# Performance work log

Hardware: AMD Instinct MI355X
Metric: run time of the kernel (lower is better)

The kernel has to match this reference:

```python
import jax, jax.numpy as jnp
import numpy as np

DELTA_V = 0.5
DELTA_D = 3.0
PARAM_VAR = 1.0
PARAM_DIST = 1.0
PARAM_REG = 0.001
NUM_BIN_LABELS = 2   # binary labels in {0,1}
NUM_INST_LABELS = 6  # background + 5 lanes


def _disc_loss_single(pred, labels, num_labels, delta_v, delta_d):
    """pred: [D, N] float, labels: [N] int in [0, num_labels).
    Assumes all labels present (true w.h.p. for large N), so
    torch.unique(sorted=True) == arange(num_labels)."""
    D, N = pred.shape
    K = num_labels
    labels = labels.astype(jnp.int32)
    ones = jnp.ones((N,), dtype=pred.dtype)
    counts = jax.ops.segment_sum(ones, labels, num_segments=K)            # [K]
    sums = jax.ops.segment_sum(pred.T, labels, num_segments=K)            # [K, D]
    means = sums / counts[:, None]                                        # [K, D] segment means

    # variance (pull) term: distance of each pixel embedding to its segment mean
    mu_expand = means[labels]                                             # [N, D]
    dist = jnp.sqrt(jnp.sum((mu_expand - pred.T) ** 2, axis=1))           # [N]
    dist = jnp.maximum(dist - delta_v, 0.0) ** 2
    var_per_label = jax.ops.segment_sum(dist, labels, num_segments=K) / counts
    l_var = jnp.mean(var_per_label)

    # distance (push) term over all ordered pairs i != j of segment means
    diff = means[:, None, :] - means[None, :, :]                          # [K, K, D]
    sq = jnp.sum(diff ** 2, axis=-1)                                      # [K, K]
    offdiag = ~jnp.eye(K, dtype=bool)
    sq_safe = jnp.where(offdiag, sq, 1.0)  # avoid sqrt(0) grad NaN on diagonal
    dn = jnp.maximum(2.0 * delta_d - jnp.sqrt(sq_safe), 0.0) ** 2
    l_dist = jnp.sum(jnp.where(offdiag, dn, 0.0)) / (K * (K - 1))

    # regularizer: mean L2 norm of segment means (norm over feature dim)
    l_reg = jnp.mean(jnp.sqrt(jnp.sum(means ** 2, axis=1)))

    return PARAM_VAR * l_var + PARAM_DIST * l_dist + PARAM_REG * l_reg


def setup_inputs() -> dict:
    key = jax.random.key(0)
    k1, k2, k3, k4 = jax.random.split(key, 4)
    B, MN = 4, 512 * 1024
    return {
        "binary_logits": jax.random.normal(k1, (B, 2, MN), dtype=jnp.float32),
        "binary_labels": jax.random.randint(k2, (B, MN), 0, NUM_BIN_LABELS, dtype=jnp.int64),
        "instance_logits": jax.random.normal(k3, (B, 5, MN), dtype=jnp.float32),
        "instance_labels": jax.random.randint(k4, (B, MN), 0, NUM_INST_LABELS, dtype=jnp.int64),
    }


def reference(binary_logits, binary_labels, instance_logits, instance_labels):
    bin_loss_per = jax.vmap(
        lambda p, l: _disc_loss_single(p, l, NUM_BIN_LABELS, DELTA_V, DELTA_D)
    )(binary_logits, binary_labels)
    inst_loss_per = jax.vmap(
        lambda p, l: _disc_loss_single(p, l, NUM_INST_LABELS, DELTA_V, DELTA_D)
    )(instance_logits, instance_labels)
    return jnp.mean(bin_loss_per), jnp.mean(inst_loss_per)
```

## Files before the change

### kernel.cpp

```cpp
#include <hip/hip_runtime.h>
#include <math.h>

#define DELTA_V 0.5f
#define DELTA_D 3.0f
#define P_REG   0.001f

#define BPS   128
#define TPB   256
#define NVMAX 36

#define P1_OFF   0
#define CNT_OFF  (8 * BPS * 36)
#define MEAN_OFF (CNT_OFF + 48)
#define LDR_OFF  (MEAN_OFF + 240)
#define P2_OFF   (LDR_OFF + 8)

template<int K, int D>
__device__ void pass1_body(const float* __restrict__ pred,
                           const int*  __restrict__ labels,
                           float* __restrict__ partials,
                           int n4, float (*lredW)[NVMAX]) {
    constexpr int NV = K * (D + 1);
    const float4* pred4 = (const float4*)pred;
    const int4*   lab4  = (const int4*)labels;

    float acc[K][D + 1];
    #pragma unroll
    for (int k = 0; k < K; ++k)
        #pragma unroll
        for (int j = 0; j <= D; ++j) acc[k][j] = 0.f;

    const int idx0   = blockIdx.x * TPB + threadIdx.x;
    const int stride = BPS * TPB;
    for (int i = idx0; i < n4; i += stride) {
        int4 lv = lab4[i];
        int labs[4] = {lv.x, lv.y, lv.z, lv.w};
        float4 xv[D];
        #pragma unroll
        for (int d = 0; d < D; ++d) xv[d] = pred4[(size_t)d * n4 + i];
        const float* xs = (const float*)&xv[0];
        #pragma unroll
        for (int c = 0; c < 4; ++c) {
            const int lab = labs[c];
            #pragma unroll
            for (int k = 0; k < K; ++k) {
                const float ind = (lab == k) ? 1.f : 0.f;
                acc[k][D] += ind;
                #pragma unroll
                for (int d = 0; d < D; ++d)
                    acc[k][d] = fmaf(ind, xs[d * 4 + c], acc[k][d]);
            }
        }
    }

    const int wave = threadIdx.x >> 6, lane = threadIdx.x & 63;
    #pragma unroll
    for (int k = 0; k < K; ++k) {
        #pragma unroll
        for (int j = 0; j <= D; ++j) {
            float v = acc[k][j];
            for (int off = 32; off > 0; off >>= 1) v += __shfl_down(v, off);
            if (lane == 0) lredW[wave][k * (D + 1) + j] = v;
        }
    }
    __syncthreads();
    if (threadIdx.x < NV) {
        const int t = threadIdx.x;
        partials[t] = lredW[0][t] + lredW[1][t] + lredW[2][t] + lredW[3][t];
    }
}

__global__ __launch_bounds__(TPB)
void pass1_fused(const float* __restrict__ bl, const int* __restrict__ bL,
                 const float* __restrict__ il, const int* __restrict__ iL,
                 float* __restrict__ ws, int MN) {
    const int s = blockIdx.y, b = s & 3;
    __shared__ float lredW[4][NVMAX];
    float* partials = ws + P1_OFF + (size_t)(s * BPS + blockIdx.x) * NVMAX;
    if (s < 4) pass1_body<2, 2>(bl + (size_t)b * 2 * MN, bL + (size_t)b * MN, partials, MN >> 2, lredW);
    else       pass1_body<6, 5>(il + (size_t)b * 5 * MN, iL + (size_t)b * MN, partials, MN >> 2, lredW);
}

__global__ void mid_kernel(float* __restrict__ ws) {
    const int s = blockIdx.x;
    const int isInst = s >> 2;
    const int K = isInst ? 6 : 2, D = isInst ? 5 : 2;
    const int NV = K * (D + 1);
    const float* P = ws + P1_OFF + (size_t)s * BPS * NVMAX;
    const int t = threadIdx.x;
    __shared__ float tot[NVMAX];
    __shared__ float muS[30];
    __shared__ float cntS[6];
    if (t < NV) {
        float v = 0.f;
        for (int j = 0; j < BPS; ++j) v += P[j * NVMAX + t];
        tot[t] = v;
        const int k = t / (D + 1), jj = t % (D + 1);
        if (jj == D) { cntS[k] = v; ws[CNT_OFF + s * 6 + k] = v; }
    }
    __syncthreads();
    if (t < NV) {
        const int k = t / (D + 1), jj = t % (D + 1);
        if (jj < D) {
            const float m = tot[t] / cntS[k];
            muS[k * D + jj] = m;
            ws[MEAN_OFF + s * 30 + k * D + jj] = m;
        }
    }
    __syncthreads();
    if (t == 0) {
        float l_dist = 0.f, l_reg = 0.f;
        for (int i = 0; i < K; ++i) {
            float n2 = 0.f;
            for (int d = 0; d < D; ++d) n2 += muS[i * D + d] * muS[i * D + d];
            l_reg += sqrtf(n2);
            for (int j = 0; j < K; ++j) {
                if (i == j) continue;
                float sq = 0.f;
                for (int d = 0; d < D; ++d) { const float df = muS[i * D + d] - muS[j * D + d]; sq += df * df; }
                const float dn = fmaxf(2.f * DELTA_D - sqrtf(sq), 0.f);
                l_dist += dn * dn;
            }
        }
        l_dist /= (float)(K * (K - 1));
        l_reg  /= (float)K;
        ws[LDR_OFF + s] = l_dist + P_REG * l_reg;
    }
}

template<int K, int D>
__device__ void pass2_body(const float* __restrict__ pred,
                           const int*  __restrict__ labels,
                           const float* __restrict__ means,
                           float* __restrict__ partials,
                           int n4, float* mu, float (*lredW)[6]) {
    if (threadIdx.x < K * D) mu[threadIdx.x] = means[threadIdx.x];
    __syncthreads();

    const float4* pred4 = (const float4*)pred;
    const int4*   lab4  = (const int4*)labels;

    float acc[K];
    #pragma unroll
    for (int k = 0; k < K; ++k) acc[k] = 0.f;

    const int idx0   = blockIdx.x * TPB + threadIdx.x;
    const int stride = BPS * TPB;
    for (int i = idx0; i < n4; i += stride) {
        int4 lv = lab4[i];
        int labs[4] = {lv.x, lv.y, lv.z, lv.w};
        float4 xv[D];
        #pragma unroll
        for (int d = 0; d < D; ++d) xv[d] = pred4[(size_t)d * n4 + i];
        const float* xs = (const float*)&xv[0];
        #pragma unroll
        for (int c = 0; c < 4; ++c) {
            const int lab = labs[c];
            float sq = 0.f;
            #pragma unroll
            for (int d = 0; d < D; ++d) {
                const float df = mu[lab * D + d] - xs[d * 4 + c];
                sq = fmaf(df, df, sq);
            }
            const float h = fmaxf(sqrtf(sq) - DELTA_V, 0.f);
            const float h2 = h * h;
            #pragma unroll
            for (int k = 0; k < K; ++k)
                acc[k] += (lab == k) ? h2 : 0.f;
        }
    }

    const int wave = threadIdx.x >> 6, lane = threadIdx.x & 63;
    #pragma unroll
    for (int k = 0; k < K; ++k) {
        float v = acc[k];
        for (int off = 32; off > 0; off >>= 1) v += __shfl_down(v, off);
        if (lane == 0) lredW[wave][k] = v;
    }
    __syncthreads();
    if (threadIdx.x < K) {
        const int t = threadIdx.x;
        partials[t] = lredW[0][t] + lredW[1][t] + lredW[2][t] + lredW[3][t];
    }
}

__global__ __launch_bounds__(TPB)
void pass2_fused(const float* __restrict__ bl, const int* __restrict__ bL,
                 const float* __restrict__ il, const int* __restrict__ iL,
                 float* __restrict__ ws, int MN) {
    const int s = blockIdx.y, b = s & 3;
    __shared__ float mu[30];
    __shared__ float lredW[4][6];
    const float* means = ws + MEAN_OFF + s * 30;
    float* partials = ws + P2_OFF + (size_t)(s * BPS + blockIdx.x) * 6;
    if (s < 4) pass2_body<2, 2>(bl + (size_t)b * 2 * MN, bL + (size_t)b * MN, means, partials, MN >> 2, mu, lredW);
    else       pass2_body<6, 5>(il + (size_t)b * 5 * MN, iL + (size_t)b * MN, means, partials, MN >> 2, mu, lredW);
}

__global__ void final_kernel(const float* __restrict__ ws, float* __restrict__ out) {
    __shared__ float contrib[48];
    const int t = threadIdx.x;
    if (t < 48) {
        const int s = t / 6, k = t % 6;
        const int Ks = (s < 4) ? 2 : 6;
        float c = 0.f;
        if (k < Ks) {
            float v = 0.f;
            for (int j = 0; j < BPS; ++j) v += ws[P2_OFF + (size_t)(s * BPS + j) * 6 + k];
            c = v / ws[CNT_OFF + s * 6 + k];
        }
        contrib[t] = c;
    }
    __syncthreads();
    if (t == 0) {
        float totB = 0.f, totI = 0.f;
        for (int s = 0; s < 8; ++s) {
            const int Ks = (s < 4) ? 2 : 6;
            float lv = 0.f;
            for (int k = 0; k < Ks; ++k) lv += contrib[s * 6 + k];
            lv /= (float)Ks;
            const float loss = lv + ws[LDR_OFF + s];
            if (s < 4) totB += loss; else totI += loss;
        }
        out[0] = totB * 0.25f;
        out[1] = totI * 0.25f;
    }
}

extern "C" void kernel_launch(void* const* d_in, const int* in_sizes, int n_in,
                              void* d_out, int out_size, void* d_ws, size_t ws_size,
                              hipStream_t stream) {
    const float* bin_logits  = (const float*)d_in[0];
    const int*   bin_labels  = (const int*)d_in[1];
    const float* inst_logits = (const float*)d_in[2];
    const int*   inst_labels = (const int*)d_in[3];
    float* ws  = (float*)d_ws;
    float* out = (float*)d_out;

    const int B  = 4;
    const int MN = in_sizes[1] / B;

    dim3 grid(BPS, 8), block(TPB);
    pass1_fused<<<grid, block, 0, stream>>>(bin_logits, bin_labels, inst_logits, inst_labels, ws, MN);
    mid_kernel<<<8, 64, 0, stream>>>(ws);
    pass2_fused<<<grid, block, 0, stream>>>(bin_logits, bin_labels, inst_logits, inst_labels, ws, MN);
    final_kernel<<<1, 64, 0, stream>>>(ws, out);
}
```

Before: 140.2 us.

## Fold mid and final reductions into passes via last-block atomic counters

Replaces the separate mid and final kernels with a last-block-done pattern. Each pass kernel increments an atomic counter, and the last block performs the cross-block reduction, which removes two small kernel launches. The grid becomes 1D and gives binary segments 64 blocks and instance segments 128 blocks, which rebalances work between the lighter and heavier segments. It adds a memset for the counters, threadfences, and an atomic per block.

```diff
diff --git a/kernel.cpp b/kernel.cpp
--- a/kernel.cpp
+++ b/kernel.cpp
@@ -5,12 +5,15 @@
 #define DELTA_D 3.0f
 #define P_REG   0.001f
 
-#define BPS   128
-#define TPB   256
-#define NVMAX 36
-
-#define P1_OFF   0
-#define CNT_OFF  (8 * BPS * 36)
+#define TPB    256
+#define BIN_B  64
+#define INST_B 128
+#define NBLK   (4 * BIN_B + 4 * INST_B)
+#define NVMAX  36
+
+#define CTR_OFF  0
+#define P1_OFF   16
+#define CNT_OFF  (P1_OFF + 8 * INST_B * NVMAX)
 #define MEAN_OFF (CNT_OFF + 48)
 #define LDR_OFF  (MEAN_OFF + 240)
 #define P2_OFF   (LDR_OFF + 8)
@@ -19,7 +22,7 @@
 __device__ void pass1_body(const float* __restrict__ pred,
                            const int*  __restrict__ labels,
                            float* __restrict__ partials,
-                           int n4, float (*lredW)[NVMAX]) {
+                           int n4, int j, int NB, float (*lredW)[NVMAX]) {
     constexpr int NV = K * (D + 1);
     const float4* pred4 = (const float4*)pred;
     const int4*   lab4  = (const int4*)labels;
@@ -28,10 +31,10 @@
     #pragma unroll
     for (int k = 0; k < K; ++k)
         #pragma unroll
-        for (int j = 0; j <= D; ++j) acc[k][j] = 0.f;
-
-    const int idx0   = blockIdx.x * TPB + threadIdx.x;
-    const int stride = BPS * TPB;
+        for (int jj = 0; jj <= D; ++jj) acc[k][jj] = 0.f;
+
+    const int idx0   = j * TPB + threadIdx.x;
+    const int stride = NB * TPB;
     for (int i = idx0; i < n4; i += stride) {
         int4 lv = lab4[i];
         int labs[4] = {lv.x, lv.y, lv.z, lv.w};
@@ -57,10 +60,10 @@
     #pragma unroll
     for (int k = 0; k < K; ++k) {
         #pragma unroll
-        for (int j = 0; j <= D; ++j) {
-            float v = acc[k][j];
+        for (int jj = 0; jj <= D; ++jj) {
+            float v = acc[k][jj];
             for (int off = 32; off > 0; off >>= 1) v += __shfl_down(v, off);
-            if (lane == 0) lredW[wave][k * (D + 1) + j] = v;
+            if (lane == 0) lredW[wave][k * (D + 1) + jj] = v;
         }
     }
     __syncthreads();
@@ -70,41 +73,57 @@
     }
 }
 
+__device__ __forceinline__ void block_map(int bx, int& s, int& j, int& NB) {
+    if (bx < 4 * BIN_B) { s = bx / BIN_B; j = bx % BIN_B; NB = BIN_B; }
+    else { int q = bx - 4 * BIN_B; s = 4 + q / INST_B; j = q % INST_B; NB = INST_B; }
+}
+
 __global__ __launch_bounds__(TPB)
-void pass1_fused(const float* __restrict__ bl, const int* __restrict__ bL,
-                 const float* __restrict__ il, const int* __restrict__ iL,
-                 float* __restrict__ ws, int MN) {
-    const int s = blockIdx.y, b = s & 3;
+void k1(const float* __restrict__ bl, const int* __restrict__ bL,
+        const float* __restrict__ il, const int* __restrict__ iL,
+        float* __restrict__ ws, int MN) {
+    int s, j, NB;
+    block_map(blockIdx.x, s, j, NB);
+    const int b = s & 3;
+    const int n4 = MN >> 2;
     __shared__ float lredW[4][NVMAX];
-    float* partials = ws + P1_OFF + (size_t)(s * BPS + blockIdx.x) * NVMAX;
-    if (s < 4) pass1_body<2, 2>(bl + (size_t)b * 2 * MN, bL + (size_t)b * MN, partials, MN >> 2, lredW);
-    else       pass1_body<6, 5>(il + (size_t)b * 5 * MN, iL + (size_t)b * MN, partials, MN >> 2, lredW);
-}
-
-__global__ void mid_kernel(float* __restrict__ ws) {
-    const int s = blockIdx.x;
-    const int isInst = s >> 2;
-    const int K = isInst ? 6 : 2, D = isInst ? 5 : 2;
+    float* partials = ws + P1_OFF + (size_t)(s * INST_B + j) * NVMAX;
+    if (s < 4) pass1_body<2, 2>(bl + (size_t)b * 2 * MN, bL + (size_t)b * MN, partials, n4, j, NB, lredW);
+    else       pass1_body<6, 5>(il + (size_t)b * 5 * MN, iL + (size_t)b * MN, partials, n4, j, NB, lredW);
+    __syncthreads();
+
+    __shared__ int amLast;
+    if (threadIdx.x == 0) {
+        __threadfence();
+        int* ctr = (int*)ws + CTR_OFF + s;
+        int old = atomicAdd(ctr, 1);
+        amLast = (old == NB - 1);
+    }
+    __syncthreads();
+    if (!amLast) return;
+    __threadfence();
+
+    const int K = (s < 4) ? 2 : 6, D = (s < 4) ? 2 : 5;
     const int NV = K * (D + 1);
-    const float* P = ws + P1_OFF + (size_t)s * BPS * NVMAX;
-    const int t = threadIdx.x;
     __shared__ float tot[NVMAX];
     __shared__ float muS[30];
     __shared__ float cntS[6];
+    const int t = threadIdx.x;
     if (t < NV) {
+        const float* P = ws + P1_OFF + (size_t)s * INST_B * NVMAX;
         float v = 0.f;
-        for (int j = 0; j < BPS; ++j) v += P[j * NVMAX + t];
+        for (int jj = 0; jj < NB; ++jj) v += P[jj * NVMAX + t];
         tot[t] = v;
-        const int k = t / (D + 1), jj = t % (D + 1);
-        if (jj == D) { cntS[k] = v; ws[CNT_OFF + s * 6 + k] = v; }
+        const int k = t / (D + 1), r = t % (D + 1);
+        if (r == D) { cntS[k] = v; ws[CNT_OFF + s * 6 + k] = v; }
     }
     __syncthreads();
     if (t < NV) {
-        const int k = t / (D + 1), jj = t % (D + 1);
-        if (jj < D) {
+        const int k = t / (D + 1), r = t % (D + 1);
+        if (r < D) {
             const float m = tot[t] / cntS[k];
-            muS[k * D + jj] = m;
-            ws[MEAN_OFF + s * 30 + k * D + jj] = m;
+            muS[k * D + r] = m;
+            ws[MEAN_OFF + s * 30 + k * D + r] = m;
         }
     }
     __syncthreads();
@@ -114,10 +133,10 @@
             float n2 = 0.f;
             for (int d = 0; d < D; ++d) n2 += muS[i * D + d] * muS[i * D + d];
             l_reg += sqrtf(n2);
-            for (int j = 0; j < K; ++j) {
-                if (i == j) continue;
+            for (int jj = 0; jj < K; ++jj) {
+                if (i == jj) continue;
                 float sq = 0.f;
-                for (int d = 0; d < D; ++d) { const float df = muS[i * D + d] - muS[j * D + d]; sq += df * df; }
+                for (int d = 0; d < D; ++d) { const float df = muS[i * D + d] - muS[jj * D + d]; sq += df * df; }
                 const float dn = fmaxf(2.f * DELTA_D - sqrtf(sq), 0.f);
                 l_dist += dn * dn;
             }
@@ -125,6 +144,7 @@
         l_dist /= (float)(K * (K - 1));
         l_reg  /= (float)K;
         ws[LDR_OFF + s] = l_dist + P_REG * l_reg;
+        __threadfence();
     }
 }
 
@@ -133,7 +153,7 @@
                            const int*  __restrict__ labels,
                            const float* __restrict__ means,
                            float* __restrict__ partials,
-                           int n4, float* mu, float (*lredW)[6]) {
+                           int n4, int j, int NB, float* mu, float (*lredW)[6]) {
     if (threadIdx.x < K * D) mu[threadIdx.x] = means[threadIdx.x];
     __syncthreads();
 
@@ -144,8 +164,8 @@
     #pragma unroll
     for (int k = 0; k < K; ++k) acc[k] = 0.f;
 
-    const int idx0   = blockIdx.x * TPB + threadIdx.x;
-    const int stride = BPS * TPB;
+    const int idx0   = j * TPB + threadIdx.x;
+    const int stride = NB * TPB;
     for (int i = idx0; i < n4; i += stride) {
         int4 lv = lab4[i];
         int labs[4] = {lv.x, lv.y, lv.z, lv.w};
@@ -185,42 +205,57 @@
 }
 
 __global__ __launch_bounds__(TPB)
-void pass2_fused(const float* __restrict__ bl, const int* __restrict__ bL,
-                 const float* __restrict__ il, const int* __restrict__ iL,
-                 float* __restrict__ ws, int MN) {
-    const int s = blockIdx.y, b = s & 3;
+void k2(const float* __restrict__ bl, const int* __restrict__ bL,
+        const float* __restrict__ il, const int* __restrict__ iL,
+        float* __restrict__ ws, float* __restrict__ out, int MN) {
+    int s, j, NB;
+    block_map(blockIdx.x, s, j, NB);
+    const int b = s & 3;
+    const int n4 = MN >> 2;
     __shared__ float mu[30];
     __shared__ float lredW[4][6];
     const float* means = ws + MEAN_OFF + s * 30;
-    float* partials = ws + P2_OFF + (size_t)(s * BPS + blockIdx.x) * 6;
-    if (s < 4) pass2_body<2, 2>(bl + (size_t)b * 2 * MN, bL + (size_t)b * MN, means, partials, MN >> 2, mu, lredW);
-    else       pass2_body<6, 5>(il + (size_t)b * 5 * MN, iL + (size_t)b * MN, means, partials, MN >> 2, mu, lredW);
-}
-
-__global__ void final_kernel(const float* __restrict__ ws, float* __restrict__ out) {
+    float* partials = ws + P2_OFF + (size_t)(s * INST_B + j) * 6;
+    if (s < 4) pass2_body<2, 2>(bl + (size_t)b * 2 * MN, bL + (size_t)b * MN, means, partials, n4, j, NB, mu, lredW);
+    else       pass2_body<6, 5>(il + (size_t)b * 5 * MN, iL + (size_t)b * MN, means, partials, n4, j, NB, mu, lredW);
+    __syncthreads();
+
+    __shared__ int amLast;
+    if (threadIdx.x == 0) {
+        __threadfence();
+        int* ctr = (int*)ws + CTR_OFF + 8;
+        int old = atomicAdd(ctr, 1);
+        amLast = (old == NBLK - 1);
+    }
+    __syncthreads();
+    if (!amLast) return;
+    __threadfence();
+
     __shared__ float contrib[48];
     const int t = threadIdx.x;
     if (t < 48) {
-        const int s = t / 6, k = t % 6;
-        const int Ks = (s < 4) ? 2 : 6;
+        const int s2 = t / 6, k = t % 6;
+        const int Ks = (s2 < 4) ? 2 : 6;
+        const int NBs = (s2 < 4) ? BIN_B : INST_B;
         float c = 0.f;
         if (k < Ks) {
+            const float* P = ws + P2_OFF + (size_t)s2 * INST_B * 6;
             float v = 0.f;
-            for (int j = 0; j < BPS; ++j) v += ws[P2_OFF + (size_t)(s * BPS + j) * 6 + k];
-            c = v / ws[CNT_OFF + s * 6 + k];
+            for (int jj = 0; jj < NBs; ++jj) v += P[jj * 6 + k];
+            c = v / ws[CNT_OFF + s2 * 6 + k];
         }
         contrib[t] = c;
     }
     __syncthreads();
     if (t == 0) {
         float totB = 0.f, totI = 0.f;
-        for (int s = 0; s < 8; ++s) {
-            const int Ks = (s < 4) ? 2 : 6;
+        for (int s2 = 0; s2 < 8; ++s2) {
+            const int Ks = (s2 < 4) ? 2 : 6;
             float lv = 0.f;
-            for (int k = 0; k < Ks; ++k) lv += contrib[s * 6 + k];
+            for (int k = 0; k < Ks; ++k) lv += contrib[s2 * 6 + k];
             lv /= (float)Ks;
-            const float loss = lv + ws[LDR_OFF + s];
-            if (s < 4) totB += loss; else totI += loss;
+            const float loss = lv + ws[LDR_OFF + s2];
+            if (s2 < 4) totB += loss; else totI += loss;
         }
         out[0] = totB * 0.25f;
         out[1] = totI * 0.25f;
@@ -240,9 +275,7 @@
     const int B  = 4;
     const int MN = in_sizes[1] / B;
 
-    dim3 grid(BPS, 8), block(TPB);
-    pass1_fused<<<grid, block, 0, stream>>>(bin_logits, bin_labels, inst_logits, inst_labels, ws, MN);
-    mid_kernel<<<8, 64, 0, stream>>>(ws);
-    pass2_fused<<<grid, block, 0, stream>>>(bin_logits, bin_labels, inst_logits, inst_labels, ws, MN);
-    final_kernel<<<1, 64, 0, stream>>>(ws, out);
-}
+    (void)hipMemsetAsync(d_ws, 0, 64, stream);
+    k1<<<NBLK, TPB, 0, stream>>>(bin_logits, bin_labels, inst_logits, inst_labels, ws, MN);
+    k2<<<NBLK, TPB, 0, stream>>>(bin_logits, bin_labels, inst_logits, inst_labels, ws, out, MN);
+}
```

After: 220.1 us. +57.0%, slower.
